# Performance work log

Measured on AMD Instinct MI355X. Metric: run time of the kernel, lower is better.

## Reference

```python
import jax, jax.numpy as jnp
import numpy as np

NHEAD = 8
GROUPS = 32   # GroupNorm(32) assumed for ConvNormActivation's norm (diffusion-UNet convention)
EPS = 1e-5


def group_norm(x, scale, bias):
    # x: [B, C, H, W]
    b, c, h, w = x.shape
    xg = x.reshape(b, GROUPS, c // GROUPS, h, w)
    mu = xg.mean(axis=(2, 3, 4), keepdims=True)
    var = xg.var(axis=(2, 3, 4), keepdims=True)
    xg = (xg - mu) * jax.lax.rsqrt(var + EPS)
    return xg.reshape(b, c, h, w) * scale[None, :, None, None] + bias[None, :, None, None]


def setup_inputs() -> dict:
    key = jax.random.key(0)
    ks = jax.random.split(key, 3)
    B, C, H, W = 8, 512, 32, 32
    s = 0.02
    return {
        "x": jax.random.normal(ks[0], (B, C, H, W), jnp.float32),
        "gn1_scale": jnp.ones((C,), jnp.float32),
        "gn1_bias": jnp.zeros((C,), jnp.float32),
        "w_qkv": jax.random.normal(ks[1], (3 * C, C), jnp.float32) * s,  # 1x1 conv kernel
        "b_qkv": jnp.zeros((3 * C,), jnp.float32),
        "w_proj": jax.random.normal(ks[2], (C, C), jnp.float32) * s,    # 1x1 conv kernel
        "b_proj": jnp.zeros((C,), jnp.float32),
        "gn2_scale": jnp.ones((C,), jnp.float32),
        "gn2_bias": jnp.zeros((C,), jnp.float32),
    }


def reference(x, gn1_scale, gn1_bias, w_qkv, b_qkv, w_proj, b_proj, gn2_scale, gn2_bias):
    b, c, h, w = x.shape
    n = h * w
    ch = c // NHEAD

    # qkv = Conv1x1(GroupNorm(x))  (norm_first=True)
    hn = group_norm(x, gn1_scale, gn1_bias)
    qkv = jnp.einsum('bchw,oc->bohw', hn, w_qkv) + b_qkv[None, :, None, None]

    # [B, 3C, H, W] -> [B*heads, 3*ch, N], split into q,k,v (matches torch reshape/split)
    qkv = qkv.reshape(b * NHEAD, 3 * ch, n)
    q, k, v = jnp.split(qkv, 3, axis=1)

    scale = ch ** -0.25
    wgt = jnp.einsum('bct,bcs->bts', q * scale, k * scale)   # [B*H, N, N]
    wgt = jax.nn.softmax(wgt, axis=-1)                        # stable (max-subtract fused)
    a = jnp.einsum('bts,bcs->bct', wgt, v).reshape(b, c, h, w)

    # proj_out = GroupNorm(Conv1x1(a))  (norm after conv, Identity activation)
    out = jnp.einsum('bchw,oc->bohw', a, w_proj) + b_proj[None, :, None, None]
    out = group_norm(out, gn2_scale, gn2_bias)
    return x + out
```

## Files before the change

### kernel.cpp

```cpp
#include <hip/hip_runtime.h>
#include <math.h>

#define NB 8
#define NC 512
#define NHW 1024
#define NG 32
#define CPG 16
#define QKV_C 1536
#define EPS 1e-5f
#define QSCALE 0.18033688011112042f

typedef float  f32x4  __attribute__((ext_vector_type(4)));
typedef __bf16 bf16x8 __attribute__((ext_vector_type(8)));
typedef __bf16 bf16x4 __attribute__((ext_vector_type(4)));
typedef short  s16x4  __attribute__((ext_vector_type(4)));

__device__ __forceinline__ void gload_lds16(const void* g, void* l) {
    __builtin_amdgcn_global_load_lds(
        (const __attribute__((address_space(1))) void*)g,
        (__attribute__((address_space(3))) void*)l, 16, 0, 0);
}

__device__ __forceinline__ void dma_drain() {
    asm volatile("s_waitcnt vmcnt(0)" ::: "memory");
}

__device__ __forceinline__ f32x4 mfma16(bf16x4 a, bf16x4 b, f32x4 c) {
#if __has_builtin(__builtin_amdgcn_mfma_f32_16x16x16bf16_1k)
    return __builtin_amdgcn_mfma_f32_16x16x16bf16_1k(
        __builtin_bit_cast(s16x4, a), __builtin_bit_cast(s16x4, b), c, 0, 0, 0);
#else
    f32x4 d;
    asm volatile("v_mfma_f32_16x16x16_bf16 %0, %1, %2, %3"
                 : "=v"(d) : "v"(a), "v"(b), "v"(c));
    return d;
#endif
}

__global__ __launch_bounds__(256) void prep_k(const float* __restrict__ x,
                                              float* __restrict__ mu,
                                              float* __restrict__ rinv,
                                              const float* __restrict__ w1,
                                              __bf16* __restrict__ d1,
                                              const float* __restrict__ w2,
                                              __bf16* __restrict__ d2,
                                              float* __restrict__ gstat) {
    const int bi = blockIdx.x;
    if (bi < 256) {
        const int grp = bi;
        const float4* p4 = (const float4*)(x + (size_t)grp * (CPG * NHW));
        float s = 0.f, s2 = 0.f;
        for (int i = threadIdx.x; i < CPG * NHW / 4; i += 256) {
            float4 v = p4[i];
            s  += v.x + v.y + v.z + v.w;
            s2 += v.x * v.x + v.y * v.y + v.z * v.z + v.w * v.w;
        }
        for (int off = 32; off > 0; off >>= 1) {
            s  += __shfl_down(s, off);
            s2 += __shfl_down(s2, off);
        }
        __shared__ float ls[4], ls2[4];
        const int wv = threadIdx.x >> 6;
        if ((threadIdx.x & 63) == 0) { ls[wv] = s; ls2[wv] = s2; }
        __syncthreads();
        if (threadIdx.x == 0) {
            float S = ls[0] + ls[1] + ls[2] + ls[3];
            float S2 = ls2[0] + ls2[1] + ls2[2] + ls2[3];
            const float inv = 1.f / (float)(CPG * NHW);
            float m = S * inv;
            float var = S2 * inv - m * m;
            mu[grp] = m;
            rinv[grp] = rsqrtf(var + EPS);
        }
        if (bi == 0 && threadIdx.x < 256) {
            gstat[threadIdx.x] = 0.f;
            gstat[threadIdx.x + 256] = 0.f;
        }
    } else {
        const int n1_4 = QKV_C * NC / 4;
        const int i = (bi - 256) * 256 + threadIdx.x;
        const float4* s = (i < n1_4) ? (const float4*)w1 + i
                                     : (const float4*)w2 + (i - n1_4);
        bf16x4* d = (i < n1_4) ? (bf16x4*)d1 + i : (bf16x4*)d2 + (i - n1_4);
        float4 v = *s;
        bf16x4 o;
        o[0] = (__bf16)v.x; o[1] = (__bf16)v.y; o[2] = (__bf16)v.z; o[3] = (__bf16)v.w;
        *d = o;
    }
}

__global__ __launch_bounds__(256) void gn_apply_t_k(const float* __restrict__ x,
                                                    const float* __restrict__ mu,
                                                    const float* __restrict__ rinv,
                                                    const float* __restrict__ sc,
                                                    const float* __restrict__ bi,
                                                    __bf16* __restrict__ hnT) {
    __shared__ float T[64][65];
    const int tid = threadIdx.x;
    const int nb = blockIdx.x * 64, cb = blockIdx.y * 64, b = blockIdx.z;
    const int col = (tid & 15) * 4;
    const int rb = tid >> 4;
    #pragma unroll
    for (int rr = 0; rr < 4; rr++) {
        int cl = rr * 16 + rb;
        int c = cb + cl;
        int grp = b * NG + (c >> 4);
        float a = sc[c] * rinv[grp];
        float d = bi[c] - mu[grp] * a;
        float4 v4 = *(const float4*)&x[((size_t)(b * NC + c)) * NHW + nb + col];
        T[cl][col + 0] = v4.x * a + d;
        T[cl][col + 1] = v4.y * a + d;
        T[cl][col + 2] = v4.z * a + d;
        T[cl][col + 3] = v4.w * a + d;
    }
    __syncthreads();
    const int nl = tid >> 2;
    const int c0 = (tid & 3) * 16;
    bf16x8 o0, o1;
    #pragma unroll
    for (int i = 0; i < 8; i++) o0[i] = (__bf16)T[c0 + i][nl];
    #pragma unroll
    for (int i = 0; i < 8; i++) o1[i] = (__bf16)T[c0 + 8 + i][nl];
    __bf16* dst = hnT + ((size_t)(b * NHW + nb + nl)) * NC + cb + c0;
    *(bf16x8*)dst = o0;
    *(bf16x8*)(dst + 8) = o1;
}

__device__ __forceinline__ void mm_stage(const __bf16* __restrict__ W,
                                         const __bf16* __restrict__ Bm,
                                         int K, int m0, int n0, int k0,
                                         __bf16* As, __bf16* Bs) {
    const int tid = threadIdx.x;
    const int w = tid >> 6, lane = tid & 63;
    const int lr = lane >> 2, lk = (lane & 3) * 8;
    #pragma unroll
    for (int i = 0; i < 2; i++) {
        int rb = (w * 2 + i) * 16;
        gload_lds16(W  + (size_t)(m0 + rb + lr) * K + k0 + lk, As + rb * 32);
        gload_lds16(Bm + (size_t)(n0 + rb + lr) * K + k0 + lk, Bs + rb * 32);
    }
}

__device__ __forceinline__ void mm_core(const __bf16* __restrict__ W,
                                        const __bf16* __restrict__ Bm,
                                        int K, int m0, int n0,
                                        __bf16* As, __bf16* Bs,
                                        f32x4 (&acc)[4][4]) {
    const int tid = threadIdx.x;
    const int w = tid >> 6, lane = tid & 63;
    const int l15 = lane & 15, quad = lane >> 4;
    const int wm = (w & 1) * 64, wn = (w >> 1) * 64;
    const int nk = K >> 5;
    mm_stage(W, Bm, K, m0, n0, 0, As, Bs);
    for (int it = 0; it < nk; it++) {
        const int cur = (it & 1) * 4096;
        dma_drain();
        __syncthreads();
        if (it + 1 < nk)
            mm_stage(W, Bm, K, m0, n0, (it + 1) * 32, As + (4096 - cur), Bs + (4096 - cur));
        bf16x8 af[4], bfv[4];
        #pragma unroll
        for (int mi = 0; mi < 4; mi++)
            af[mi] = *(const bf16x8*)(As + cur + (wm + mi * 16 + l15) * 32 + quad * 8);
        #pragma unroll
        for (int ni = 0; ni < 4; ni++)
            bfv[ni] = *(const bf16x8*)(Bs + cur + (wn + ni * 16 + l15) * 32 + quad * 8);
        #pragma unroll
        for (int mi = 0; mi < 4; mi++)
            #pragma unroll
            for (int ni = 0; ni < 4; ni++)
                acc[mi][ni] = __builtin_amdgcn_mfma_f32_16x16x32_bf16(
                    af[mi], bfv[ni], acc[mi][ni], 0, 0, 0);
    }
}

__global__ __launch_bounds__(256) void qkv_gemm_k(const __bf16* __restrict__ W,
                                                  const __bf16* __restrict__ hnT,
                                                  const float* __restrict__ bias,
                                                  __bf16* __restrict__ qT,
                                                  __bf16* __restrict__ kT,
                                                  __bf16* __restrict__ v) {
    __shared__ __bf16 As[2 * 128 * 32];
    __shared__ __bf16 Bs[2 * 128 * 32];
    const int m0 = blockIdx.x * 128, n0 = blockIdx.y * 128, b = blockIdx.z;
    f32x4 acc[4][4] = {};
    mm_core(W, hnT + (size_t)b * NHW * NC, NC, m0, n0, As, Bs, acc);
    const int tid = threadIdx.x;
    const int w = tid >> 6, lane = tid & 63;
    const int l15 = lane & 15, quad = lane >> 4;
    const int wm = (w & 1) * 64, wn = (w >> 1) * 64;
    #pragma unroll
    for (int mi = 0; mi < 4; mi++) {
        const int mbase = m0 + wm + mi * 16 + quad * 4;
        const f32x4 bb4 = *(const f32x4*)&bias[mbase];
        const int h = mbase / 192;
        const int rr = mbase - h * 192;
        const int bh = b * 8 + h;
        #pragma unroll
        for (int ni = 0; ni < 4; ni++) {
            const int n = n0 + wn + ni * 16 + l15;
            f32x4 a4 = acc[mi][ni];
            if (rr < 64) {
                bf16x4 o;
                #pragma unroll
                for (int r = 0; r < 4; r++) o[r] = (__bf16)((a4[r] + bb4[r]) * QSCALE);
                *(bf16x4*)&qT[((size_t)bh << 16) + n * 64 + rr] = o;
            } else if (rr < 128) {
                bf16x4 o;
                #pragma unroll
                for (int r = 0; r < 4; r++) o[r] = (__bf16)(a4[r] + bb4[r]);
                *(bf16x4*)&kT[((size_t)bh << 16) + n * 64 + (rr - 64)] = o;
            } else {
                #pragma unroll
                for (int r = 0; r < 4; r++)
                    v[((size_t)(bh * 64 + rr - 128 + r)) * NHW + n] = (__bf16)(a4[r] + bb4[r]);
            }
        }
    }
}

__global__ __launch_bounds__(256) void proj_gemm_k(const __bf16* __restrict__ W,
                                                   const __bf16* __restrict__ aTin,
                                                   const float* __restrict__ bias,
                                                   __bf16* __restrict__ projb,
                                                   float* __restrict__ gstat) {
    __shared__ __bf16 As[2 * 64 * 32];
    __shared__ __bf16 Bs[2 * 128 * 32];
    const int m0 = blockIdx.x * 64, n0 = blockIdx.y * 128, b = blockIdx.z;
    const __bf16* Bm = aTin + (size_t)b * NHW * NC;
    const int tid = threadIdx.x;
    const int w = tid >> 6, lane = tid & 63;
    const int l15 = lane & 15, quad = lane >> 4;
    const int lr = lane >> 2, lk = (lane & 3) * 8;
    f32x4 acc[4][2] = {};
    {
        gload_lds16(W + (size_t)(m0 + w * 16 + lr) * NC + lk, As + (w * 16) * 32);
        #pragma unroll
        for (int i = 0; i < 2; i++) {
            int rb = w * 32 + i * 16;
            gload_lds16(Bm + (size_t)(n0 + rb + lr) * NC + lk, Bs + rb * 32);
        }
    }
    for (int it = 0; it < 16; it++) {
        const int curA = (it & 1) * 2048, curB = (it & 1) * 4096;
        dma_drain();
        __syncthreads();
        if (it + 1 < 16) {
            const int k0 = (it + 1) * 32;
            gload_lds16(W + (size_t)(m0 + w * 16 + lr) * NC + k0 + lk,
                        As + (2048 - curA) + (w * 16) * 32);
            #pragma unroll
            for (int i = 0; i < 2; i++) {
                int rb = w * 32 + i * 16;
                gload_lds16(Bm + (size_t)(n0 + rb + lr) * NC + k0 + lk,
                            Bs + (4096 - curB) + rb * 32);
            }
        }
        bf16x8 af[4], bfv[2];
        #pragma unroll
        for (int mi = 0; mi < 4; mi++)
            af[mi] = *(const bf16x8*)(As + curA + (mi * 16 + l15) * 32 + quad * 8);
        #pragma unroll
        for (int ni = 0; ni < 2; ni++)
            bfv[ni] = *(const bf16x8*)(Bs + curB + (w * 32 + ni * 16 + l15) * 32 + quad * 8);
        #pragma unroll
        for (int mi = 0; mi < 4; mi++)
            #pragma unroll
            for (int ni = 0; ni < 2; ni++)
                acc[mi][ni] = __builtin_amdgcn_mfma_f32_16x16x32_bf16(
                    af[mi], bfv[ni], acc[mi][ni], 0, 0, 0);
    }
    float bsum[4] = {}, bsq[4] = {};
    #pragma unroll
    for (int mi = 0; mi < 4; mi++) {
        #pragma unroll
        for (int r = 0; r < 4; r++) {
            int m = m0 + mi * 16 + quad * 4 + r;
            float bb = bias[m];
            #pragma unroll
            for (int ni = 0; ni < 2; ni++) {
                int n = n0 + w * 32 + ni * 16 + l15;
                float val = acc[mi][ni][r] + bb;
                projb[((size_t)(b * NC + m)) * NHW + n] = (__bf16)val;
                bsum[mi] += val;
                bsq[mi] += val * val;
            }
        }
    }
    #pragma unroll
    for (int mi = 0; mi < 4; mi++) {
        float s = bsum[mi], q = bsq[mi];
        #pragma unroll
        for (int off = 1; off < 64; off <<= 1) {
            s += __shfl_xor(s, off);
            q += __shfl_xor(q, off);
        }
        if (lane == 0) {
            int grp = b * NG + (m0 >> 4) + mi;
            atomicAdd(&gstat[grp], s);
            atomicAdd(&gstat[256 + grp], q);
        }
    }
}

__global__ __launch_bounds__(256) void attn_k(const __bf16* __restrict__ qT,
                                              const __bf16* __restrict__ kT,
                                              const __bf16* __restrict__ vv,
                                              __bf16* __restrict__ aT) {
    __shared__ __align__(16) char smem[32768];
    __bf16* Kt = (__bf16*)smem;
    __bf16* Vt = (__bf16*)(smem + 16384);
    float*  Om = (float*)smem;
    float*  Lr = (float*)(smem + 17408);
    const int tid = threadIdx.x;
    const int w = tid >> 6, lane = tid & 63;
    const int l15 = lane & 15, quad = lane >> 4;
    const int lr = lane >> 2, lk = (lane & 3) * 8;
    const int bh = blockIdx.x, t0 = blockIdx.y * 64;
    const __bf16* qb = qT + ((size_t)bh << 16);
    const __bf16* kb = kT + ((size_t)bh << 16);
    const __bf16* vb = vv + ((size_t)bh << 6) * NHW;
    const int xmask = l15 & 14;

    bf16x8 qfr[4][2];
    #pragma unroll
    for (int tb = 0; tb < 4; tb++)
        #pragma unroll
        for (int ch = 0; ch < 2; ch++)
            qfr[tb][ch] = *(const bf16x8*)(qb + (size_t)(t0 + tb * 16 + l15) * 64
                                           + ch * 32 + quad * 8);
    #pragma unroll
    for (int i = 0; i < 4; i++) {
        int inst = w * 4 + i;
        if (inst < 8) {
            int ch = inst >> 2, sb = (inst & 3) * 16;
            gload_lds16(kb + (size_t)(sb + lr) * 64 + ch * 32 + lk,
                        Kt + ch * 2048 + sb * 32);
        } else {
            int ip = inst - 8;
            int c = ip * 8 + (lane >> 3);
            int m2 = (lane & 7) * 2;
            gload_lds16(vb + (size_t)c * NHW + 4 * (m2 ^ (c & 14)),
                        Vt + ip * 512);
        }
    }
    float lp[4] = {};
    f32x4 Oacc[4][4] = {};

    for (int it = 0; it < 16; it++) {
        const int cur = (it & 1) * 4096;
        const int nxt = 4096 - cur;
        dma_drain();
        __syncthreads();
        if (it + 1 < 16) {
            const int s0 = (it + 1) * 64;
            #pragma unroll
            for (int i = 0; i < 4; i++) {
                int inst = w * 4 + i;
                if (inst < 8) {
                    int ch = inst >> 2, sb = (inst & 3) * 16;
                    gload_lds16(kb + (size_t)(s0 + sb + lr) * 64 + ch * 32 + lk,
                                Kt + nxt + ch * 2048 + sb * 32);
                } else {
                    int ip = inst - 8;
                    int c = ip * 8 + (lane >> 3);
                    int m2 = (lane & 7) * 2;
                    gload_lds16(vb + (size_t)c * NHW + s0 + 4 * (m2 ^ (c & 14)),
                                Vt + nxt + ip * 512);
                }
            }
        }
        f32x4 sacc[4] = {};
        #pragma unroll
        for (int ch = 0; ch < 2; ch++) {
            bf16x8 kfr = *(const bf16x8*)(Kt + cur + ch * 2048
                                          + (w * 16 + l15) * 32 + quad * 8);
            #pragma unroll
            for (int tb = 0; tb < 4; tb++)
                sacc[tb] = __builtin_amdgcn_mfma_f32_16x16x32_bf16(
                    kfr, qfr[tb][ch], sacc[tb], 0, 0, 0);
        }
        bf16x4 pf[4];
        #pragma unroll
        for (int tb = 0; tb < 4; tb++) {
            bf16x4 pk;
            #pragma unroll
            for (int r = 0; r < 4; r++) {
                float pv = __builtin_amdgcn_exp2f(sacc[tb][r]);
                lp[tb] += pv;
                pk[r] = (__bf16)pv;
            }
            pf[tb] = pk;
        }
        #pragma unroll
        for (int ci = 0; ci < 4; ci++) {
            bf16x4 vfr = *(const bf16x4*)(Vt + cur + (((w * 4 + quad) ^ xmask) << 2)
                                          + (ci * 16 + l15) * 64);
            #pragma unroll
            for (int tb = 0; tb < 4; tb++)
                Oacc[tb][ci] = mfma16(pf[tb], vfr, Oacc[tb][ci]);
        }
    }
    float lsum[4];
    #pragma unroll
    for (int tb = 0; tb < 4; tb++) {
        float s = lp[tb];
        s += __shfl_xor(s, 16);
        s += __shfl_xor(s, 32);
        lsum[tb] = s;
    }
    __syncthreads();
    #pragma unroll
    for (int ph = 0; ph < 4; ph++) {
        if (w == ph) {
            #pragma unroll
            for (int tb = 0; tb < 4; tb++) {
                #pragma unroll
                for (int ci = 0; ci < 4; ci++) {
                    float* dst = Om + (ci * 16 + l15) * 68 + tb * 16 + quad * 4;
                    f32x4 val = Oacc[tb][ci];
                    if (ph) val += *(const f32x4*)dst;
                    *(f32x4*)dst = val;
                }
                if (quad == 0) {
                    float* lt = Lr + tb * 16 + l15;
                    *lt = (ph ? *lt : 0.f) + lsum[tb];
                }
            }
        }
        __syncthreads();
    }
    const int b = bh >> 3, hh = bh & 7;
    const int t = tid >> 2, cb2 = (tid & 3) * 16;
    const float linv = 1.f / Lr[t];
    bf16x8 o0, o1;
    #pragma unroll
    for (int i = 0; i < 8; i++) o0[i] = (__bf16)(Om[(cb2 + i) * 68 + t] * linv);
    #pragma unroll
    for (int i = 0; i < 8; i++) o1[i] = (__bf16)(Om[(cb2 + 8 + i) * 68 + t] * linv);
    __bf16* dst = aT + ((size_t)(b * NHW + t0 + t)) * NC + hh * 64 + cb2;
    *(bf16x8*)dst = o0;
    *(bf16x8*)(dst + 8) = o1;
}

__global__ __launch_bounds__(256) void final_k(const float* __restrict__ x,
                                               const __bf16* __restrict__ pb,
                                               const float* __restrict__ gstat,
                                               const float* __restrict__ sc,
                                               const float* __restrict__ bi,
                                               float* __restrict__ out) {
    const int i4 = blockIdx.x * 256 + threadIdx.x;
    const int c  = (i4 >> 8) & (NC - 1);
    const int b  = i4 >> 17;
    const int grp = b * NG + (c >> 4);
    const float inv = 1.f / (float)(CPG * NHW);
    const float m = gstat[grp] * inv;
    const float var = gstat[256 + grp] * inv - m * m;
    const float r = rsqrtf(var + EPS);
    const float a = sc[c] * r;
    const float d = bi[c] - m * a;
    float4 xv = ((const float4*)x)[i4];
    bf16x4 pv = ((const bf16x4*)pb)[i4];
    float4 o = make_float4(xv.x + (float)pv[0] * a + d, xv.y + (float)pv[1] * a + d,
                           xv.z + (float)pv[2] * a + d, xv.w + (float)pv[3] * a + d);
    ((float4*)out)[i4] = o;
}

extern "C" void kernel_launch(void* const* d_in, const int* in_sizes, int n_in,
                              void* d_out, int out_size, void* d_ws, size_t ws_size,
                              hipStream_t stream) {
    const float* x      = (const float*)d_in[0];
    const float* gn1_s  = (const float*)d_in[1];
    const float* gn1_b  = (const float*)d_in[2];
    const float* w_qkv  = (const float*)d_in[3];
    const float* b_qkv  = (const float*)d_in[4];
    const float* w_proj = (const float*)d_in[5];
    const float* b_proj = (const float*)d_in[6];
    const float* gn2_s  = (const float*)d_in[7];
    const float* gn2_b  = (const float*)d_in[8];
    float* out = (float*)d_out;

    char* p = (char*)d_ws;
    __bf16* hnT   = (__bf16*)p;           p += (size_t)8 * 1024 * 512 * 2;
    __bf16* qT    = (__bf16*)p;           p += (size_t)64 * 1024 * 64 * 2;
    __bf16* kT    = (__bf16*)p;           p += (size_t)64 * 1024 * 64 * 2;
    __bf16* vB    = (__bf16*)p;           p += (size_t)64 * 64 * 1024 * 2;
    __bf16* aT    = (__bf16*)p;           p += (size_t)8 * 1024 * 512 * 2;
    __bf16* projb = (__bf16*)p;           p += (size_t)8 * 512 * 1024 * 2;
    __bf16* wq    = (__bf16*)p;           p += (size_t)QKV_C * NC * 2;
    __bf16* wp    = (__bf16*)p;           p += (size_t)NC * NC * 2;
    float*  mu1   = (float*)p;            p += 256 * 4;
    float*  ri1   = (float*)p;            p += 256 * 4;
    float*  gstat = (float*)p;            p += 512 * 4;

    prep_k<<<1280, 256, 0, stream>>>(x, mu1, ri1, w_qkv, wq, w_proj, wp, gstat);
    gn_apply_t_k<<<dim3(16, 8, 8), 256, 0, stream>>>(x, mu1, ri1, gn1_s, gn1_b, hnT);

    qkv_gemm_k<<<dim3(12, 8, 8), 256, 0, stream>>>(wq, hnT, b_qkv, qT, kT, vB);

    attn_k<<<dim3(64, 16), 256, 0, stream>>>(qT, kT, vB, aT);

    proj_gemm_k<<<dim3(8, 8, 8), 256, 0, stream>>>(wp, aT, b_proj, projb, gstat);

    final_k<<<4096, 256, 0, stream>>>(x, projb, gstat, gn2_s, gn2_b, out);
}
```

Measured before the change: 187.1 us.

## Split attention work by query rows per wave instead of key columns

Each attention block now handles 128 query rows, with each wave owning 32 of them, and walks the key/value sequence in 128-wide tiles. Previously each wave owned a slice of the keys, so partial outputs had to be summed across waves through shared memory before normalising. Now every wave holds complete output rows and writes them straight to global memory, which removes the four-phase LDS reduction and its barriers and halves the number of blocks. In exchange, K/V LDS use doubles to 64KB, fewer blocks are launched (512 instead of 1024), and the final stores are scattered 2-byte writes that are not coalesced.

```diff
diff --git a/kernel.cpp b/kernel.cpp
--- a/kernel.cpp
+++ b/kernel.cpp
@@ -307,140 +307,123 @@
                                               const __bf16* __restrict__ kT,
                                               const __bf16* __restrict__ vv,
                                               __bf16* __restrict__ aT) {
-    __shared__ __align__(16) char smem[32768];
-    __bf16* Kt = (__bf16*)smem;
-    __bf16* Vt = (__bf16*)(smem + 16384);
-    float*  Om = (float*)smem;
-    float*  Lr = (float*)(smem + 17408);
+    __shared__ __bf16 Kt[2 * 8192];
+    __shared__ __bf16 Vt[2 * 8192];
     const int tid = threadIdx.x;
     const int w = tid >> 6, lane = tid & 63;
     const int l15 = lane & 15, quad = lane >> 4;
     const int lr = lane >> 2, lk = (lane & 3) * 8;
-    const int bh = blockIdx.x, t0 = blockIdx.y * 64;
+    const int bh = blockIdx.x, t0 = blockIdx.y * 128;
     const __bf16* qb = qT + ((size_t)bh << 16);
     const __bf16* kb = kT + ((size_t)bh << 16);
     const __bf16* vb = vv + ((size_t)bh << 6) * NHW;
     const int xmask = l15 & 14;
 
-    bf16x8 qfr[4][2];
-    #pragma unroll
-    for (int tb = 0; tb < 4; tb++)
+    bf16x8 qfr[2][2];
+    #pragma unroll
+    for (int tb = 0; tb < 2; tb++)
         #pragma unroll
         for (int ch = 0; ch < 2; ch++)
-            qfr[tb][ch] = *(const bf16x8*)(qb + (size_t)(t0 + tb * 16 + l15) * 64
+            qfr[tb][ch] = *(const bf16x8*)(qb + (size_t)(t0 + w * 32 + tb * 16 + l15) * 64
                                            + ch * 32 + quad * 8);
     #pragma unroll
-    for (int i = 0; i < 4; i++) {
-        int inst = w * 4 + i;
-        if (inst < 8) {
-            int ch = inst >> 2, sb = (inst & 3) * 16;
+    for (int i = 0; i < 8; i++) {
+        int inst = w * 8 + i;
+        if (inst < 16) {
+            int ch = inst >> 3, sb = (inst & 7) * 16;
             gload_lds16(kb + (size_t)(sb + lr) * 64 + ch * 32 + lk,
-                        Kt + ch * 2048 + sb * 32);
+                        Kt + ch * 4096 + sb * 32);
         } else {
-            int ip = inst - 8;
-            int c = ip * 8 + (lane >> 3);
-            int m2 = (lane & 7) * 2;
+            int ip = inst - 16;
+            int c = ip * 4 + (lane >> 4);
+            int m2 = (lane & 15) * 2;
             gload_lds16(vb + (size_t)c * NHW + 4 * (m2 ^ (c & 14)),
                         Vt + ip * 512);
         }
     }
-    float lp[4] = {};
-    f32x4 Oacc[4][4] = {};
-
-    for (int it = 0; it < 16; it++) {
-        const int cur = (it & 1) * 4096;
-        const int nxt = 4096 - cur;
+    float lp[2] = {0.f, 0.f};
+    f32x4 Oacc[2][4] = {};
+
+    for (int it = 0; it < 8; it++) {
+        const int cur = (it & 1) * 8192;
+        const int nxt = 8192 - cur;
         dma_drain();
         __syncthreads();
-        if (it + 1 < 16) {
-            const int s0 = (it + 1) * 64;
-            #pragma unroll
-            for (int i = 0; i < 4; i++) {
-                int inst = w * 4 + i;
-                if (inst < 8) {
-                    int ch = inst >> 2, sb = (inst & 3) * 16;
+        if (it + 1 < 8) {
+            const int s0 = (it + 1) * 128;
+            #pragma unroll
+            for (int i = 0; i < 8; i++) {
+                int inst = w * 8 + i;
+                if (inst < 16) {
+                    int ch = inst >> 3, sb = (inst & 7) * 16;
                     gload_lds16(kb + (size_t)(s0 + sb + lr) * 64 + ch * 32 + lk,
-                                Kt + nxt + ch * 2048 + sb * 32);
+                                Kt + nxt + ch * 4096 + sb * 32);
                 } else {
-                    int ip = inst - 8;
-                    int c = ip * 8 + (lane >> 3);
-                    int m2 = (lane & 7) * 2;
+                    int ip = inst - 16;
+                    int c = ip * 4 + (lane >> 4);
+                    int m2 = (lane & 15) * 2;
                     gload_lds16(vb + (size_t)c * NHW + s0 + 4 * (m2 ^ (c & 14)),
                                 Vt + nxt + ip * 512);
                 }
             }
         }
-        f32x4 sacc[4] = {};
-        #pragma unroll
-        for (int ch = 0; ch < 2; ch++) {
-            bf16x8 kfr = *(const bf16x8*)(Kt + cur + ch * 2048
-                                          + (w * 16 + l15) * 32 + quad * 8);
-            #pragma unroll
-            for (int tb = 0; tb < 4; tb++)
-                sacc[tb] = __builtin_amdgcn_mfma_f32_16x16x32_bf16(
-                    kfr, qfr[tb][ch], sacc[tb], 0, 0, 0);
-        }
-        bf16x4 pf[4];
-        #pragma unroll
-        for (int tb = 0; tb < 4; tb++) {
-            bf16x4 pk;
-            #pragma unroll
-            for (int r = 0; r < 4; r++) {
-                float pv = __builtin_amdgcn_exp2f(sacc[tb][r]);
-                lp[tb] += pv;
-                pk[r] = (__bf16)pv;
+        #pragma unroll
+        for (int h = 0; h < 2; h++) {
+            f32x4 sacc[2][4] = {};
+            #pragma unroll
+            for (int ch = 0; ch < 2; ch++)
+                #pragma unroll
+                for (int j = 0; j < 4; j++) {
+                    bf16x8 kfr = *(const bf16x8*)(Kt + cur + ch * 4096
+                                                  + (h * 64 + j * 16 + l15) * 32 + quad * 8);
+                    sacc[0][j] = __builtin_amdgcn_mfma_f32_16x16x32_bf16(
+                        kfr, qfr[0][ch], sacc[0][j], 0, 0, 0);
+                    sacc[1][j] = __builtin_amdgcn_mfma_f32_16x16x32_bf16(
+                        kfr, qfr[1][ch], sacc[1][j], 0, 0, 0);
+                }
+            bf16x4 pf[2][4];
+            #pragma unroll
+            for (int tb = 0; tb < 2; tb++)
+                #pragma unroll
+                for (int j = 0; j < 4; j++) {
+                    bf16x4 pk;
+                    #pragma unroll
+                    for (int r = 0; r < 4; r++) {
+                        float pv = __builtin_amdgcn_exp2f(sacc[tb][j][r]);
+                        lp[tb] += pv;
+                        pk[r] = (__bf16)pv;
+                    }
+                    pf[tb][j] = pk;
+                }
+            #pragma unroll
+            for (int jt = 0; jt < 4; jt++) {
+                const __bf16* vbase = Vt + cur
+                    + ((h * 16 + ((jt * 4 + quad) ^ xmask)) << 2);
+                #pragma unroll
+                for (int ci = 0; ci < 4; ci++) {
+                    bf16x4 vfr = *(const bf16x4*)(vbase + (ci * 16 + l15) * 128);
+                    Oacc[0][ci] = mfma16(pf[0][jt], vfr, Oacc[0][ci]);
+                    Oacc[1][ci] = mfma16(pf[1][jt], vfr, Oacc[1][ci]);
+                }
             }
-            pf[tb] = pk;
-        }
-        #pragma unroll
-        for (int ci = 0; ci < 4; ci++) {
-            bf16x4 vfr = *(const bf16x4*)(Vt + cur + (((w * 4 + quad) ^ xmask) << 2)
-                                          + (ci * 16 + l15) * 64);
-            #pragma unroll
-            for (int tb = 0; tb < 4; tb++)
-                Oacc[tb][ci] = mfma16(pf[tb], vfr, Oacc[tb][ci]);
-        }
-    }
-    float lsum[4];
-    #pragma unroll
-    for (int tb = 0; tb < 4; tb++) {
+        }
+    }
+    const int b = bh >> 3, hh = bh & 7;
+    #pragma unroll
+    for (int tb = 0; tb < 2; tb++) {
         float s = lp[tb];
         s += __shfl_xor(s, 16);
         s += __shfl_xor(s, 32);
-        lsum[tb] = s;
-    }
-    __syncthreads();
-    #pragma unroll
-    for (int ph = 0; ph < 4; ph++) {
-        if (w == ph) {
-            #pragma unroll
-            for (int tb = 0; tb < 4; tb++) {
-                #pragma unroll
-                for (int ci = 0; ci < 4; ci++) {
-                    float* dst = Om + (ci * 16 + l15) * 68 + tb * 16 + quad * 4;
-                    f32x4 val = Oacc[tb][ci];
-                    if (ph) val += *(const f32x4*)dst;
-                    *(f32x4*)dst = val;
-                }
-                if (quad == 0) {
-                    float* lt = Lr + tb * 16 + l15;
-                    *lt = (ph ? *lt : 0.f) + lsum[tb];
-                }
-            }
-        }
-        __syncthreads();
-    }
-    const int b = bh >> 3, hh = bh & 7;
-    const int t = tid >> 2, cb2 = (tid & 3) * 16;
-    const float linv = 1.f / Lr[t];
-    bf16x8 o0, o1;
-    #pragma unroll
-    for (int i = 0; i < 8; i++) o0[i] = (__bf16)(Om[(cb2 + i) * 68 + t] * linv);
-    #pragma unroll
-    for (int i = 0; i < 8; i++) o1[i] = (__bf16)(Om[(cb2 + 8 + i) * 68 + t] * linv);
-    __bf16* dst = aT + ((size_t)(b * NHW + t0 + t)) * NC + hh * 64 + cb2;
-    *(bf16x8*)dst = o0;
-    *(bf16x8*)(dst + 8) = o1;
+        #pragma unroll
+        for (int r = 0; r < 4; r++) {
+            float inv = 1.f / __shfl(s, quad * 4 + r);
+            int t = t0 + w * 32 + tb * 16 + quad * 4 + r;
+            size_t base = ((size_t)(b * NHW + t)) * NC + hh * 64;
+            #pragma unroll
+            for (int ci = 0; ci < 4; ci++)
+                aT[base + ci * 16 + l15] = (__bf16)(Oacc[tb][ci][r] * inv);
+        }
+    }
 }
 
 __global__ __launch_bounds__(256) void final_k(const float* __restrict__ x,
@@ -498,7 +481,7 @@
 
     qkv_gemm_k<<<dim3(12, 8, 8), 256, 0, stream>>>(wq, hnT, b_qkv, qT, kT, vB);
 
-    attn_k<<<dim3(64, 16), 256, 0, stream>>>(qT, kT, vB, aT);
+    attn_k<<<dim3(64, 8), 256, 0, stream>>>(qT, kT, vB, aT);
 
     proj_gemm_k<<<dim3(8, 8, 8), 256, 0, stream>>>(wp, aT, b_proj, projb, gstat);
 
```

Result: faster. 176.4 us (-5.7%).

## Split attention work by query rows per wave instead of key columns

Applied to the files above, without the earlier changes.

Each wave now owns 16 query rows and iterates over all 64 keys of each tile, instead of owning 16 keys for all 64 queries. This removes the cross-wave reduction of partial O accumulators and row sums through shared memory, the four serialized sync phases, and the LDS transpose before the store. Register pressure drops (4 accumulators instead of 16), and launch bounds request 4 blocks per SM for occupancy. Each wave now reads the full K and V tiles from LDS, which raises LDS read traffic.

```diff
diff --git a/kernel.cpp b/kernel.cpp
--- a/kernel.cpp
+++ b/kernel.cpp
@@ -303,15 +303,12 @@
     }
 }
 
-__global__ __launch_bounds__(256) void attn_k(const __bf16* __restrict__ qT,
-                                              const __bf16* __restrict__ kT,
-                                              const __bf16* __restrict__ vv,
-                                              __bf16* __restrict__ aT) {
-    __shared__ __align__(16) char smem[32768];
-    __bf16* Kt = (__bf16*)smem;
-    __bf16* Vt = (__bf16*)(smem + 16384);
-    float*  Om = (float*)smem;
-    float*  Lr = (float*)(smem + 17408);
+__global__ __launch_bounds__(256, 4) void attn_k(const __bf16* __restrict__ qT,
+                                                 const __bf16* __restrict__ kT,
+                                                 const __bf16* __restrict__ vv,
+                                                 __bf16* __restrict__ aT) {
+    __shared__ __bf16 Kt[2 * 4096];
+    __shared__ __bf16 Vt[2 * 4096];
     const int tid = threadIdx.x;
     const int w = tid >> 6, lane = tid & 63;
     const int l15 = lane & 15, quad = lane >> 4;
@@ -322,13 +319,11 @@
     const __bf16* vb = vv + ((size_t)bh << 6) * NHW;
     const int xmask = l15 & 14;
 
-    bf16x8 qfr[4][2];
-    #pragma unroll
-    for (int tb = 0; tb < 4; tb++)
-        #pragma unroll
-        for (int ch = 0; ch < 2; ch++)
-            qfr[tb][ch] = *(const bf16x8*)(qb + (size_t)(t0 + tb * 16 + l15) * 64
-                                           + ch * 32 + quad * 8);
+    bf16x8 qfr[2];
+    #pragma unroll
+    for (int ch = 0; ch < 2; ch++)
+        qfr[ch] = *(const bf16x8*)(qb + (size_t)(t0 + w * 16 + l15) * 64
+                                   + ch * 32 + quad * 8);
     #pragma unroll
     for (int i = 0; i < 4; i++) {
         int inst = w * 4 + i;
@@ -344,8 +339,8 @@
                         Vt + ip * 512);
         }
     }
-    float lp[4] = {};
-    f32x4 Oacc[4][4] = {};
+    float lp = 0.f;
+    f32x4 Oacc[4] = {};
 
     for (int it = 0; it < 16; it++) {
         const int cur = (it & 1) * 4096;
@@ -372,75 +367,50 @@
         }
         f32x4 sacc[4] = {};
         #pragma unroll
-        for (int ch = 0; ch < 2; ch++) {
-            bf16x8 kfr = *(const bf16x8*)(Kt + cur + ch * 2048
-                                          + (w * 16 + l15) * 32 + quad * 8);
-            #pragma unroll
-            for (int tb = 0; tb < 4; tb++)
-                sacc[tb] = __builtin_amdgcn_mfma_f32_16x16x32_bf16(
-                    kfr, qfr[tb][ch], sacc[tb], 0, 0, 0);
-        }
+        for (int ch = 0; ch < 2; ch++)
+            #pragma unroll
+            for (int j = 0; j < 4; j++) {
+                bf16x8 kfr = *(const bf16x8*)(Kt + cur + ch * 2048
+                                              + (j * 16 + l15) * 32 + quad * 8);
+                sacc[j] = __builtin_amdgcn_mfma_f32_16x16x32_bf16(
+                    kfr, qfr[ch], sacc[j], 0, 0, 0);
+            }
         bf16x4 pf[4];
         #pragma unroll
-        for (int tb = 0; tb < 4; tb++) {
+        for (int j = 0; j < 4; j++) {
             bf16x4 pk;
             #pragma unroll
             for (int r = 0; r < 4; r++) {
-                float pv = __builtin_amdgcn_exp2f(sacc[tb][r]);
-                lp[tb] += pv;
+                float pv = __builtin_amdgcn_exp2f(sacc[j][r]);
+                lp += pv;
                 pk[r] = (__bf16)pv;
             }
-            pf[tb] = pk;
-        }
-        #pragma unroll
-        for (int ci = 0; ci < 4; ci++) {
-            bf16x4 vfr = *(const bf16x4*)(Vt + cur + (((w * 4 + quad) ^ xmask) << 2)
-                                          + (ci * 16 + l15) * 64);
-            #pragma unroll
-            for (int tb = 0; tb < 4; tb++)
-                Oacc[tb][ci] = mfma16(pf[tb], vfr, Oacc[tb][ci]);
-        }
-    }
-    float lsum[4];
-    #pragma unroll
-    for (int tb = 0; tb < 4; tb++) {
-        float s = lp[tb];
-        s += __shfl_xor(s, 16);
-        s += __shfl_xor(s, 32);
-        lsum[tb] = s;
-    }
-    __syncthreads();
-    #pragma unroll
-    for (int ph = 0; ph < 4; ph++) {
-        if (w == ph) {
-            #pragma unroll
-            for (int tb = 0; tb < 4; tb++) {
-                #pragma unroll
-                for (int ci = 0; ci < 4; ci++) {
-                    float* dst = Om + (ci * 16 + l15) * 68 + tb * 16 + quad * 4;
-                    f32x4 val = Oacc[tb][ci];
-                    if (ph) val += *(const f32x4*)dst;
-                    *(f32x4*)dst = val;
-                }
-                if (quad == 0) {
-                    float* lt = Lr + tb * 16 + l15;
-                    *lt = (ph ? *lt : 0.f) + lsum[tb];
-                }
-            }
-        }
-        __syncthreads();
+            pf[j] = pk;
+        }
+        #pragma unroll
+        for (int jt = 0; jt < 4; jt++) {
+            const __bf16* vbase = Vt + cur + (((jt * 4 + quad) ^ xmask) << 2);
+            #pragma unroll
+            for (int ci = 0; ci < 4; ci++) {
+                bf16x4 vfr = *(const bf16x4*)(vbase + (ci * 16 + l15) * 64);
+                Oacc[ci] = mfma16(vfr, pf[jt], Oacc[ci]);
+            }
+        }
     }
     const int b = bh >> 3, hh = bh & 7;
-    const int t = tid >> 2, cb2 = (tid & 3) * 16;
-    const float linv = 1.f / Lr[t];
-    bf16x8 o0, o1;
-    #pragma unroll
-    for (int i = 0; i < 8; i++) o0[i] = (__bf16)(Om[(cb2 + i) * 68 + t] * linv);
-    #pragma unroll
-    for (int i = 0; i < 8; i++) o1[i] = (__bf16)(Om[(cb2 + 8 + i) * 68 + t] * linv);
-    __bf16* dst = aT + ((size_t)(b * NHW + t0 + t)) * NC + hh * 64 + cb2;
-    *(bf16x8*)dst = o0;
-    *(bf16x8*)(dst + 8) = o1;
+    float s = lp;
+    s += __shfl_xor(s, 16);
+    s += __shfl_xor(s, 32);
+    const float inv = 1.f / s;
+    const int t = t0 + w * 16 + l15;
+    __bf16* dst = aT + ((size_t)(b * NHW + t)) * NC + hh * 64;
+    #pragma unroll
+    for (int ci = 0; ci < 4; ci++) {
+        bf16x4 o;
+        #pragma unroll
+        for (int r = 0; r < 4; r++) o[r] = (__bf16)(Oacc[ci][r] * inv);
+        *(bf16x4*)(dst + ci * 16 + quad * 4) = o;
+    }
 }
 
 __global__ __launch_bounds__(256) void final_k(const float* __restrict__ x,
```

Measured after the change: 177.3 us. 5.2% less time.
